# Kernel optimization log

Hardware: AMD Instinct MI355X
Metric: run time of the kernel (lower is better)

Reference implementation:

```python
import jax, jax.numpy as jnp
import numpy as np

B, T, D, K = 8, 4096, 512, 4096


def setup_inputs() -> dict:
    key = jax.random.key(0)
    k1, k2 = jax.random.split(key)
    x = jax.random.normal(k1, (B, T, D), dtype=jnp.float32)
    embed = jax.random.normal(k2, (K, D), dtype=jnp.float32)
    return {"x": x, "embed": embed}


def reference(x, embed):
    # F.normalize(x, p=2, dim=-1) with eps clamp like torch (eps=1e-12)
    norm = jnp.sqrt(jnp.sum(x * x, axis=-1, keepdims=True))
    xn = x / jnp.maximum(norm, 1e-12)

    flat = xn.reshape(-1, D)  # [(B*T), D]
    x_sq = jnp.sum(flat * flat, axis=1, keepdims=True)           # [(B*T), 1]
    e_sq = jnp.sum(embed * embed, axis=1)[None, :]               # [1, K]
    dist = -(x_sq - 2.0 * (flat @ embed.T) + e_sq)               # [(B*T), K]
    embed_ind = jnp.argmax(dist, axis=-1).reshape(B, T)          # [B, T]

    # decode: embedding gather then 'b n d -> b d n'
    quantize = embed[embed_ind]                                  # [B, T, D]
    quantize = jnp.transpose(quantize, (0, 2, 1))                # [B, D, T]
    return embed_ind, quantize
```

## Files before the change

### kernel.cpp

```cpp
#include <hip/hip_runtime.h>
#include <math.h>

#define BB 8
#define TT 4096
#define DDIM 512
#define KK 4096
#define NN (BB*TT)
#define EPS 0.05f

typedef __attribute__((ext_vector_type(8))) short bf16x8;
typedef __attribute__((ext_vector_type(4))) float f32x4;

__device__ __forceinline__ void async16(void* lds, const void* g) {
  __builtin_amdgcn_global_load_lds((const __attribute__((address_space(1))) void*)g,
                                   (__attribute__((address_space(3))) void*)lds, 16, 0, 0);
}

__device__ __forceinline__ unsigned pk_bf16(float a, float b) {
  unsigned ua = __float_as_uint(a); ua += 0x7FFFu + ((ua >> 16) & 1u);
  unsigned ub = __float_as_uint(b); ub += 0x7FFFu + ((ub >> 16) & 1u);
  return (ua >> 16) | (ub & 0xFFFF0000u);
}

__global__ __launch_bounds__(256) void prep_kernel(const float* __restrict__ src,
                                                   short* __restrict__ dst16,
                                                   float* __restrict__ outv, int mode) {
  int r = blockIdx.x * 4 + (threadIdx.x >> 6);
  int lane = threadIdx.x & 63;
  const float4* row4 = (const float4*)(src + (size_t)r * DDIM);
  float4 v0 = row4[lane];
  float4 v1 = row4[lane + 64];
  uint2 p0, p1;
  p0.x = pk_bf16(v0.x, v0.y); p0.y = pk_bf16(v0.z, v0.w);
  p1.x = pk_bf16(v1.x, v1.y); p1.y = pk_bf16(v1.z, v1.w);
  *(uint2*)(dst16 + (size_t)r * DDIM + lane * 4) = p0;
  *(uint2*)(dst16 + (size_t)r * DDIM + 256 + lane * 4) = p1;
  float ss = v0.x*v0.x + v0.y*v0.y + v0.z*v0.z + v0.w*v0.w
           + v1.x*v1.x + v1.y*v1.y + v1.z*v1.z + v1.w*v1.w;
  #pragma unroll
  for (int off = 32; off; off >>= 1) ss += __shfl_down(ss, off);
  if (lane == 0) outv[r] = mode ? 2.0f / fmaxf(sqrtf(ss), 1e-12f) : ss;
}

__global__ __launch_bounds__(256, 2) void vq_mfma(const short* __restrict__ xb,
                                                  const short* __restrict__ eb,
                                                  const float* __restrict__ esq,
                                                  const float* __restrict__ inv2,
                                                  float4* __restrict__ top2) {
  __shared__ short As[128 * 64];
  __shared__ short Bs[128 * 64];
  __shared__ float rS1[2][128];
  __shared__ float rS2[2][128];
  __shared__ int   rI1[2][128];

  const int tid = threadIdx.x;
  const int lane = tid & 63;
  const int w = tid >> 6;
  const int wr = w >> 1, wc = w & 1;
  const int q = lane >> 4, c16 = lane & 15;

  const int mb = blockIdx.x & 255;
  const int kq = blockIdx.x >> 8;
  const int n0 = mb * 128;
  const int kbase = kq * 1024;

  const int srow = w * 32 + (lane >> 3);
  const int scol = ((lane & 7) ^ (lane >> 3)) * 8;
  const short* gA = xb + (size_t)(n0 + srow) * DDIM + scol;

  float s1[16], s2v[16];
  int   i1[16];
  #pragma unroll
  for (int s = 0; s < 16; ++s) { s1[s] = -3e38f; s2v[s] = -3e38f; i1[s] = 0; }

  float4 inv4[4];
  #pragma unroll
  for (int ti = 0; ti < 4; ++ti)
    inv4[ti] = *(const float4*)&inv2[n0 + wr * 64 + ti * 16 + q * 4];

  for (int c = 0; c < 8; ++c) {
    const int k0c = kbase + c * 128;
    const short* gB = eb + (size_t)(k0c + srow) * DDIM + scol;
    f32x4 acc[4][4];
    #pragma unroll
    for (int ti = 0; ti < 4; ++ti)
      #pragma unroll
      for (int tj = 0; tj < 4; ++tj) acc[ti][tj] = (f32x4){0.f, 0.f, 0.f, 0.f};

    for (int d0 = 0; d0 < DDIM; d0 += 64) {
      #pragma unroll
      for (int i = 0; i < 4; ++i) {
        async16(As + (w * 32 + i * 8) * 64, gA + (size_t)i * 8 * DDIM + d0);
        async16(Bs + (w * 32 + i * 8) * 64, gB + (size_t)i * 8 * DDIM + d0);
      }
      __syncthreads();
      #pragma unroll
      for (int ks = 0; ks < 2; ++ks) {
        const int ko = (((ks << 2) | q) ^ (lane & 7)) << 3;
        bf16x8 af[4], bf[4];
        #pragma unroll
        for (int ti = 0; ti < 4; ++ti)
          af[ti] = *(const bf16x8*)&As[(wr * 64 + ti * 16 + c16) * 64 + ko];
        #pragma unroll
        for (int tj = 0; tj < 4; ++tj)
          bf[tj] = *(const bf16x8*)&Bs[(wc * 64 + tj * 16 + c16) * 64 + ko];
        #pragma unroll
        for (int ti = 0; ti < 4; ++ti)
          #pragma unroll
          for (int tj = 0; tj < 4; ++tj)
            acc[ti][tj] = __builtin_amdgcn_mfma_f32_16x16x32_bf16(af[ti], bf[tj], acc[ti][tj], 0, 0, 0);
      }
      __syncthreads();
    }
    #pragma unroll
    for (int tj = 0; tj < 4; ++tj) {
      const int col = k0c + wc * 64 + tj * 16 + c16;
      const float nes = -esq[col];
      #pragma unroll
      for (int ti = 0; ti < 4; ++ti)
        #pragma unroll
        for (int r = 0; r < 4; ++r) {
          int slot = ti * 4 + r;
          float sc = fmaf(acc[ti][tj][r], inv4[ti][r], nes);
          float mn = fminf(sc, s1[slot]);
          s2v[slot] = fmaxf(s2v[slot], mn);
          if (sc > s1[slot]) { s1[slot] = sc; i1[slot] = col; }
        }
    }
  }

  #pragma unroll
  for (int slot = 0; slot < 16; ++slot) {
    float a1 = s1[slot], a2 = s2v[slot]; int ai = i1[slot];
    #pragma unroll
    for (int off = 1; off < 16; off <<= 1) {
      float b1 = __shfl_xor(a1, off);
      float b2 = __shfl_xor(a2, off);
      int   bi = __shfl_xor(ai, off);
      float mn = fminf(a1, b1);
      a2 = fmaxf(fmaxf(a2, b2), mn);
      if (b1 > a1 || (b1 == a1 && bi < ai)) { a1 = b1; ai = bi; }
    }
    if (c16 == 0) {
      int row = wr * 64 + (slot >> 2) * 16 + q * 4 + (slot & 3);
      rS1[wc][row] = a1; rS2[wc][row] = a2; rI1[wc][row] = ai;
    }
  }
  __syncthreads();
  if (tid < 128) {
    float a1 = rS1[0][tid], a2 = rS2[0][tid]; int ai = rI1[0][tid];
    float b1 = rS1[1][tid], b2 = rS2[1][tid]; int bi = rI1[1][tid];
    float mn = fminf(a1, b1);
    a2 = fmaxf(fmaxf(a2, b2), mn);
    if (b1 > a1 || (b1 == a1 && bi < ai)) { a1 = b1; ai = bi; }
    top2[(size_t)kq * NN + n0 + tid] = make_float4(a1, __int_as_float(ai), a2, 0.f);
  }
}

__global__ __launch_bounds__(256) void finalize_kernel(const float4* __restrict__ top2,
                                                       float* __restrict__ out_ind,
                                                       int* __restrict__ flags,
                                                       int* __restrict__ list,
                                                       int* __restrict__ cnt) {
  int row = blockIdx.x * 256 + threadIdx.x;
  float a1 = -3e38f, a2 = -3e38f; int ai = 0;
  #pragma unroll
  for (int kq = 0; kq < 4; ++kq) {
    float4 t = top2[(size_t)kq * NN + row];
    float b1 = t.x, b2 = t.z; int bi = __float_as_int(t.y);
    float mn = fminf(a1, b1);
    a2 = fmaxf(fmaxf(a2, b2), mn);
    if (b1 > a1 || (b1 == a1 && bi < ai)) { a1 = b1; ai = bi; }
  }
  out_ind[row] = (float)ai;
  if (a1 - a2 < EPS) {
    int p = atomicAdd(cnt, 1);
    list[p] = row;
    flags[row] = p + 1;
  } else {
    flags[row] = 0;
  }
}

__global__ __launch_bounds__(256) void cleanup_kernel(const float* __restrict__ x,
                                                      const float* __restrict__ embed,
                                                      const float* __restrict__ esq,
                                                      const float* __restrict__ inv2,
                                                      const int* __restrict__ list,
                                                      const int* __restrict__ cnt,
                                                      float2* __restrict__ exact) {
  __shared__ float xr[DDIM];
  __shared__ float red_s[4];
  __shared__ int   red_i[4];
  const int rs = blockIdx.x & 31, kc = blockIdx.x >> 5;
  const int tid = threadIdx.x;
  const int lane = tid & 63, wid = tid >> 6;
  const int n = *cnt;
  for (int ii = rs; ii < n; ii += 32) {
    const int row = list[ii];
    __syncthreads();
    if (tid < 128) *(float4*)&xr[tid * 4] = *(const float4*)&x[(size_t)row * DDIM + tid * 4];
    __syncthreads();
    const float iv = inv2[row];
    float bs = -3e38f; int bi = 0;
    for (int cc = 0; cc < 2; ++cc) {
      const int code = kc * 512 + cc * 256 + tid;
      const float4* er = (const float4*)&embed[(size_t)code * DDIM];
      float acc = 0.f;
      for (int d = 0; d < DDIM / 4; ++d) {
        float4 e4 = er[d];
        float4 x4 = *(const float4*)&xr[d * 4];
        acc += x4.x * e4.x + x4.y * e4.y + x4.z * e4.z + x4.w * e4.w;
      }
      float sc = fmaf(acc, iv, -esq[code]);
      if (sc > bs || (sc == bs && code < bi)) { bs = sc; bi = code; }
    }
    #pragma unroll
    for (int off = 1; off < 64; off <<= 1) {
      float b1 = __shfl_xor(bs, off);
      int   b2 = __shfl_xor(bi, off);
      if (b1 > bs || (b1 == bs && b2 < bi)) { bs = b1; bi = b2; }
    }
    if (lane == 0) { red_s[wid] = bs; red_i[wid] = bi; }
    __syncthreads();
    if (tid == 0) {
      for (int ww = 1; ww < 4; ++ww)
        if (red_s[ww] > red_s[0] || (red_s[ww] == red_s[0] && red_i[ww] < red_i[0])) {
          red_s[0] = red_s[ww]; red_i[0] = red_i[ww];
        }
      exact[(size_t)ii * 8 + kc] = make_float2(red_s[0], (float)red_i[0]);
    }
  }
}

__global__ __launch_bounds__(256) void gather_kernel(const float* __restrict__ embed,
                                                     const int* __restrict__ flags,
                                                     const float2* __restrict__ exact,
                                                     float* __restrict__ out_ind,
                                                     float* __restrict__ out_q) {
  __shared__ int lidx[64];
  __shared__ float trans[64 * 65];
  const int n0 = blockIdx.x * 64;
  const int tid = threadIdx.x;
  if (tid < 64) {
    const int row = n0 + tid;
    const int f = flags[row];
    int idx;
    if (f) {
      float bsv = -3e38f; int bi = 0;
      const float2* e8 = &exact[(size_t)(f - 1) * 8];
      #pragma unroll
      for (int k = 0; k < 8; ++k) {
        float2 t = e8[k];
        int ci = (int)t.y;
        if (t.x > bsv || (t.x == bsv && ci < bi)) { bsv = t.x; bi = ci; }
      }
      idx = bi;
      out_ind[row] = (float)idx;
    } else {
      idx = (int)out_ind[row];
    }
    lidx[tid] = idx;
  }
  __syncthreads();
  const int bb = n0 >> 12;
  const int t0 = n0 & (TT - 1);
  const int w = tid >> 6, lane = tid & 63;
  for (int d0 = 0; d0 < DDIM; d0 += 64) {
    if (d0) __syncthreads();
    #pragma unroll
    for (int qq = 0; qq < 16; ++qq) {
      int tt2 = w * 16 + qq;
      int e = lidx[tt2];
      trans[lane * 65 + tt2] = embed[(size_t)e * DDIM + d0 + lane];
    }
    __syncthreads();
    #pragma unroll
    for (int qq = 0; qq < 4; ++qq) {
      int dl = (tid >> 4) * 4 + qq;
      int t4 = (tid & 15) * 4;
      float4 o;
      o.x = trans[dl * 65 + t4 + 0];
      o.y = trans[dl * 65 + t4 + 1];
      o.z = trans[dl * 65 + t4 + 2];
      o.w = trans[dl * 65 + t4 + 3];
      *(float4*)&out_q[((size_t)bb * DDIM + d0 + dl) * TT + t0 + t4] = o;
    }
  }
}

extern "C" void kernel_launch(void* const* d_in, const int* in_sizes, int n_in,
                              void* d_out, int out_size, void* d_ws, size_t ws_size,
                              hipStream_t stream) {
  const float* x     = (const float*)d_in[0];
  const float* embed = (const float*)d_in[1];
  char* ws = (char*)d_ws;
  short* xb      = (short*)(ws);
  short* eb      = (short*)(ws + 33554432);
  float* esq     = (float*)(ws + 37748736);
  float* inv2    = (float*)(ws + 37765120);
  float4* top2   = (float4*)(ws + 37896192);
  int* list      = (int*)(ws + 39993344);
  int* flags     = (int*)(ws + 40124416);
  float2* exact  = (float2*)(ws + 40255488);
  int* cnt       = (int*)(ws + 42352640);

  float* out_ind = (float*)d_out;
  float* out_q   = out_ind + NN;

  prep_kernel<<<KK / 4, 256, 0, stream>>>(embed, eb, esq, 0);
  prep_kernel<<<NN / 4, 256, 0, stream>>>(x, xb, inv2, 1);
  hipMemsetAsync(cnt, 0, 4, stream);
  vq_mfma<<<1024, 256, 0, stream>>>(xb, eb, esq, inv2, top2);
  finalize_kernel<<<NN / 256, 256, 0, stream>>>(top2, out_ind, flags, list, cnt);
  cleanup_kernel<<<256, 256, 0, stream>>>(x, embed, esq, inv2, list, cnt, exact);
  gather_kernel<<<NN / 64, 256, 0, stream>>>(embed, flags, exact, out_ind, out_q);
}
```

Before: 326.9 us.

## Widen MFMA codebook tile, batch cleanup rows, and merge prep launches

```diff
diff --git a/kernel.cpp b/kernel.cpp
--- a/kernel.cpp
+++ b/kernel.cpp
@@ -7,6 +7,7 @@
 #define KK 4096
 #define NN (BB*TT)
 #define EPS 0.05f
+#define CMAX 16384
 
 typedef __attribute__((ext_vector_type(8))) short bf16x8;
 typedef __attribute__((ext_vector_type(4))) float f32x4;
@@ -22,10 +23,22 @@
   return (ua >> 16) | (ub & 0xFFFF0000u);
 }
 
-__global__ __launch_bounds__(256) void prep_kernel(const float* __restrict__ src,
-                                                   short* __restrict__ dst16,
-                                                   float* __restrict__ outv, int mode) {
-  int r = blockIdx.x * 4 + (threadIdx.x >> 6);
+__global__ __launch_bounds__(256) void prep_kernel(const float* __restrict__ x,
+                                                   const float* __restrict__ embed,
+                                                   short* __restrict__ xb,
+                                                   short* __restrict__ eb,
+                                                   float* __restrict__ inv2,
+                                                   float* __restrict__ esq,
+                                                   int* __restrict__ cnt) {
+  if (blockIdx.x == 0 && threadIdx.x == 0) *cnt = 0;
+  const float* src; short* dst; float* outv; int r; int mode;
+  if (blockIdx.x < KK / 4) {
+    src = embed; dst = eb; outv = esq; mode = 0;
+    r = blockIdx.x * 4 + (threadIdx.x >> 6);
+  } else {
+    src = x; dst = xb; outv = inv2; mode = 1;
+    r = (blockIdx.x - KK / 4) * 4 + (threadIdx.x >> 6);
+  }
   int lane = threadIdx.x & 63;
   const float4* row4 = (const float4*)(src + (size_t)r * DDIM);
   float4 v0 = row4[lane];
@@ -33,8 +46,8 @@
   uint2 p0, p1;
   p0.x = pk_bf16(v0.x, v0.y); p0.y = pk_bf16(v0.z, v0.w);
   p1.x = pk_bf16(v1.x, v1.y); p1.y = pk_bf16(v1.z, v1.w);
-  *(uint2*)(dst16 + (size_t)r * DDIM + lane * 4) = p0;
-  *(uint2*)(dst16 + (size_t)r * DDIM + 256 + lane * 4) = p1;
+  *(uint2*)(dst + (size_t)r * DDIM + lane * 4) = p0;
+  *(uint2*)(dst + (size_t)r * DDIM + 256 + lane * 4) = p1;
   float ss = v0.x*v0.x + v0.y*v0.y + v0.z*v0.z + v0.w*v0.w
            + v1.x*v1.x + v1.y*v1.y + v1.z*v1.z + v1.w*v1.w;
   #pragma unroll
@@ -48,7 +61,7 @@
                                                   const float* __restrict__ inv2,
                                                   float4* __restrict__ top2) {
   __shared__ short As[128 * 64];
-  __shared__ short Bs[128 * 64];
+  __shared__ short Bs[256 * 64];
   __shared__ float rS1[2][128];
   __shared__ float rS2[2][128];
   __shared__ int   rI1[2][128];
@@ -64,57 +77,63 @@
   const int n0 = mb * 128;
   const int kbase = kq * 1024;
 
-  const int srow = w * 32 + (lane >> 3);
-  const int scol = ((lane & 7) ^ (lane >> 3)) * 8;
-  const short* gA = xb + (size_t)(n0 + srow) * DDIM + scol;
+  const int srow = lane >> 3;
+  const int scol = ((lane & 7) ^ srow) * 8;
+  const short* gA = xb + (size_t)(n0 + w * 32 + srow) * DDIM + scol;
 
   float s1[16], s2v[16];
   int   i1[16];
   #pragma unroll
   for (int s = 0; s < 16; ++s) { s1[s] = -3e38f; s2v[s] = -3e38f; i1[s] = 0; }
 
-  float4 inv4[4];
+  f32x4 inv4[4];
   #pragma unroll
   for (int ti = 0; ti < 4; ++ti)
-    inv4[ti] = *(const float4*)&inv2[n0 + wr * 64 + ti * 16 + q * 4];
-
-  for (int c = 0; c < 8; ++c) {
-    const int k0c = kbase + c * 128;
-    const short* gB = eb + (size_t)(k0c + srow) * DDIM + scol;
-    f32x4 acc[4][4];
+    inv4[ti] = *(const f32x4*)&inv2[n0 + wr * 64 + ti * 16 + q * 4];
+
+  for (int c = 0; c < 4; ++c) {
+    const int k0c = kbase + c * 256;
+    const short* gB = eb + (size_t)(k0c + w * 64 + srow) * DDIM + scol;
+    f32x4 acc[4][8];
     #pragma unroll
     for (int ti = 0; ti < 4; ++ti)
       #pragma unroll
-      for (int tj = 0; tj < 4; ++tj) acc[ti][tj] = (f32x4){0.f, 0.f, 0.f, 0.f};
+      for (int tj = 0; tj < 8; ++tj) acc[ti][tj] = (f32x4){0.f, 0.f, 0.f, 0.f};
 
     for (int d0 = 0; d0 < DDIM; d0 += 64) {
       #pragma unroll
-      for (int i = 0; i < 4; ++i) {
+      for (int i = 0; i < 4; ++i)
         async16(As + (w * 32 + i * 8) * 64, gA + (size_t)i * 8 * DDIM + d0);
-        async16(Bs + (w * 32 + i * 8) * 64, gB + (size_t)i * 8 * DDIM + d0);
-      }
+      #pragma unroll
+      for (int i = 0; i < 8; ++i)
+        async16(Bs + (w * 64 + i * 8) * 64, gB + (size_t)i * 8 * DDIM + d0);
       __syncthreads();
       #pragma unroll
       for (int ks = 0; ks < 2; ++ks) {
         const int ko = (((ks << 2) | q) ^ (lane & 7)) << 3;
-        bf16x8 af[4], bf[4];
+        bf16x8 af[4];
         #pragma unroll
         for (int ti = 0; ti < 4; ++ti)
           af[ti] = *(const bf16x8*)&As[(wr * 64 + ti * 16 + c16) * 64 + ko];
         #pragma unroll
-        for (int tj = 0; tj < 4; ++tj)
-          bf[tj] = *(const bf16x8*)&Bs[(wc * 64 + tj * 16 + c16) * 64 + ko];
-        #pragma unroll
-        for (int ti = 0; ti < 4; ++ti)
+        for (int h = 0; h < 2; ++h) {
+          bf16x8 bf[4];
           #pragma unroll
-          for (int tj = 0; tj < 4; ++tj)
-            acc[ti][tj] = __builtin_amdgcn_mfma_f32_16x16x32_bf16(af[ti], bf[tj], acc[ti][tj], 0, 0, 0);
+          for (int j = 0; j < 4; ++j)
+            bf[j] = *(const bf16x8*)&Bs[(wc * 128 + (h * 4 + j) * 16 + c16) * 64 + ko];
+          #pragma unroll
+          for (int ti = 0; ti < 4; ++ti)
+            #pragma unroll
+            for (int j = 0; j < 4; ++j)
+              acc[ti][h * 4 + j] = __builtin_amdgcn_mfma_f32_16x16x32_bf16(
+                  af[ti], bf[j], acc[ti][h * 4 + j], 0, 0, 0);
+        }
       }
       __syncthreads();
     }
     #pragma unroll
-    for (int tj = 0; tj < 4; ++tj) {
-      const int col = k0c + wc * 64 + tj * 16 + c16;
+    for (int tj = 0; tj < 8; ++tj) {
+      const int col = k0c + wc * 128 + tj * 16 + c16;
       const float nes = -esq[col];
       #pragma unroll
       for (int ti = 0; ti < 4; ++ti)
@@ -173,13 +192,12 @@
     if (b1 > a1 || (b1 == a1 && bi < ai)) { a1 = b1; ai = bi; }
   }
   out_ind[row] = (float)ai;
+  int f = 0;
   if (a1 - a2 < EPS) {
     int p = atomicAdd(cnt, 1);
-    list[p] = row;
-    flags[row] = p + 1;
-  } else {
-    flags[row] = 0;
-  }
+    if (p < CMAX) { list[p] = row; f = p + 1; }
+  }
+  flags[row] = f;
 }
 
 __global__ __launch_bounds__(256) void cleanup_kernel(const float* __restrict__ x,
@@ -189,46 +207,69 @@
                                                       const int* __restrict__ list,
                                                       const int* __restrict__ cnt,
                                                       float2* __restrict__ exact) {
-  __shared__ float xr[DDIM];
-  __shared__ float red_s[4];
-  __shared__ int   red_i[4];
-  const int rs = blockIdx.x & 31, kc = blockIdx.x >> 5;
+  __shared__ float xr[16][DDIM];
+  __shared__ float xiv[16];
+  __shared__ int   rid[16];
+  __shared__ float red_s[4][16];
+  __shared__ int   red_i[4][16];
+  const int kc = blockIdx.x >> 5;
+  const int slot = blockIdx.x & 31;
   const int tid = threadIdx.x;
-  const int lane = tid & 63, wid = tid >> 6;
-  const int n = *cnt;
-  for (int ii = rs; ii < n; ii += 32) {
-    const int row = list[ii];
-    __syncthreads();
-    if (tid < 128) *(float4*)&xr[tid * 4] = *(const float4*)&x[(size_t)row * DDIM + tid * 4];
-    __syncthreads();
-    const float iv = inv2[row];
-    float bs = -3e38f; int bi = 0;
-    for (int cc = 0; cc < 2; ++cc) {
-      const int code = kc * 512 + cc * 256 + tid;
-      const float4* er = (const float4*)&embed[(size_t)code * DDIM];
-      float acc = 0.f;
-      for (int d = 0; d < DDIM / 4; ++d) {
-        float4 e4 = er[d];
-        float4 x4 = *(const float4*)&xr[d * 4];
-        acc += x4.x * e4.x + x4.y * e4.y + x4.z * e4.z + x4.w * e4.w;
-      }
-      float sc = fmaf(acc, iv, -esq[code]);
-      if (sc > bs || (sc == bs && code < bi)) { bs = sc; bi = code; }
-    }
-    #pragma unroll
-    for (int off = 1; off < 64; off <<= 1) {
-      float b1 = __shfl_xor(bs, off);
-      int   b2 = __shfl_xor(bi, off);
-      if (b1 > bs || (b1 == bs && b2 < bi)) { bs = b1; bi = b2; }
-    }
-    if (lane == 0) { red_s[wid] = bs; red_i[wid] = bi; }
-    __syncthreads();
-    if (tid == 0) {
-      for (int ww = 1; ww < 4; ++ww)
-        if (red_s[ww] > red_s[0] || (red_s[ww] == red_s[0] && red_i[ww] < red_i[0])) {
-          red_s[0] = red_s[ww]; red_i[0] = red_i[ww];
-        }
-      exact[(size_t)ii * 8 + kc] = make_float2(red_s[0], (float)red_i[0]);
+  const int lane = tid & 63, w = tid >> 6;
+  int n = *cnt; if (n > CMAX) n = CMAX;
+  const int code = kc * 256 + tid;
+  const float4* erow = (const float4*)&embed[(size_t)code * DDIM];
+  const float nes = -esq[code];
+
+  for (int tile = slot; tile * 16 < n; tile += 32) {
+    __syncthreads();
+    if (tid < 16) {
+      int pos = tile * 16 + tid;
+      int row = (pos < n) ? list[pos] : list[0];
+      rid[tid] = row;
+      xiv[tid] = inv2[row];
+    }
+    __syncthreads();
+    #pragma unroll
+    for (int i = 0; i < 8; ++i) {
+      int idx = tid + i * 256;
+      int rl = idx >> 7, d4 = idx & 127;
+      ((float4*)xr[rl])[d4] = *(const float4*)&x[(size_t)rid[rl] * DDIM + d4 * 4];
+    }
+    __syncthreads();
+    float acc[16];
+    #pragma unroll
+    for (int r = 0; r < 16; ++r) acc[r] = 0.f;
+    for (int d4 = 0; d4 < 128; ++d4) {
+      float4 e4 = erow[d4];
+      #pragma unroll
+      for (int r = 0; r < 16; ++r) {
+        float4 x4 = ((const float4*)xr[r])[d4];
+        acc[r] += e4.x * x4.x + e4.y * x4.y + e4.z * x4.z + e4.w * x4.w;
+      }
+    }
+    #pragma unroll
+    for (int r = 0; r < 16; ++r) {
+      float bs = fmaf(acc[r], xiv[r], nes);
+      int bi = code;
+      #pragma unroll
+      for (int off = 1; off < 64; off <<= 1) {
+        float b1 = __shfl_xor(bs, off);
+        int   b2 = __shfl_xor(bi, off);
+        if (b1 > bs || (b1 == bs && b2 < bi)) { bs = b1; bi = b2; }
+      }
+      if (lane == 0) { red_s[w][r] = bs; red_i[w][r] = bi; }
+    }
+    __syncthreads();
+    if (tid < 16) {
+      float bs = red_s[0][tid]; int bi = red_i[0][tid];
+      #pragma unroll
+      for (int ww = 1; ww < 4; ++ww) {
+        float b1 = red_s[ww][tid]; int b2 = red_i[ww][tid];
+        if (b1 > bs || (b1 == bs && b2 < bi)) { bs = b1; bi = b2; }
+      }
+      int pos = tile * 16 + tid;
+      if (pos < n) exact[(size_t)pos * 16 + kc] = make_float2(bs, (float)bi);
     }
   }
 }
@@ -248,10 +289,10 @@
     int idx;
     if (f) {
       float bsv = -3e38f; int bi = 0;
-      const float2* e8 = &exact[(size_t)(f - 1) * 8];
-      #pragma unroll
-      for (int k = 0; k < 8; ++k) {
-        float2 t = e8[k];
+      const float2* e16 = &exact[(size_t)(f - 1) * 16];
+      #pragma unroll
+      for (int k = 0; k < 16; ++k) {
+        float2 t = e16[k];
         int ci = (int)t.y;
         if (t.x > bsv || (t.x == bsv && ci < bi)) { bsv = t.x; bi = ci; }
       }
@@ -301,18 +342,16 @@
   float* inv2    = (float*)(ws + 37765120);
   float4* top2   = (float4*)(ws + 37896192);
   int* list      = (int*)(ws + 39993344);
-  int* flags     = (int*)(ws + 40124416);
-  float2* exact  = (float2*)(ws + 40255488);
-  int* cnt       = (int*)(ws + 42352640);
+  int* flags     = (int*)(ws + 40058880);
+  float2* exact  = (float2*)(ws + 40189952);
+  int* cnt       = (int*)(ws + 42287104);
 
   float* out_ind = (float*)d_out;
   float* out_q   = out_ind + NN;
 
-  prep_kernel<<<KK / 4, 256, 0, stream>>>(embed, eb, esq, 0);
-  prep_kernel<<<NN / 4, 256, 0, stream>>>(x, xb, inv2, 1);
-  hipMemsetAsync(cnt, 0, 4, stream);
+  prep_kernel<<<KK / 4 + NN / 4, 256, 0, stream>>>(x, embed, xb, eb, inv2, esq, cnt);
   vq_mfma<<<1024, 256, 0, stream>>>(xb, eb, esq, inv2, top2);
   finalize_kernel<<<NN / 256, 256, 0, stream>>>(top2, out_ind, flags, list, cnt);
-  cleanup_kernel<<<256, 256, 0, stream>>>(x, embed, esq, inv2, list, cnt, exact);
+  cleanup_kernel<<<512, 256, 0, stream>>>(x, embed, esq, inv2, list, cnt, exact);
   gather_kernel<<<NN / 64, 256, 0, stream>>>(embed, flags, exact, out_ind, out_q);
 }
```

Measured after the change: 348.7 us. +6.7%, slower.

## Fuse finalize, cleanup and gather into one tail kernel with per-chunk candidate rescoring

Applied to the files above, without the earlier changes.

```diff
diff --git a/kernel.cpp b/kernel.cpp
--- a/kernel.cpp
+++ b/kernel.cpp
@@ -6,7 +6,8 @@
 #define DDIM 512
 #define KK 4096
 #define NN (BB*TT)
-#define EPS 0.05f
+#define EPS 0.035f
+#define LCAP 2048
 
 typedef __attribute__((ext_vector_type(8))) short bf16x8;
 typedef __attribute__((ext_vector_type(4))) float f32x4;
@@ -22,10 +23,20 @@
   return (ua >> 16) | (ub & 0xFFFF0000u);
 }
 
-__global__ __launch_bounds__(256) void prep_kernel(const float* __restrict__ src,
-                                                   short* __restrict__ dst16,
-                                                   float* __restrict__ outv, int mode) {
-  int r = blockIdx.x * 4 + (threadIdx.x >> 6);
+__global__ __launch_bounds__(256) void prep_kernel(const float* __restrict__ x,
+                                                   const float* __restrict__ embed,
+                                                   short* __restrict__ xb,
+                                                   short* __restrict__ eb,
+                                                   float* __restrict__ inv2,
+                                                   float* __restrict__ esq) {
+  const float* src; short* dst; float* outv; int r; int mode;
+  if (blockIdx.x < KK / 4) {
+    src = embed; dst = eb; outv = esq; mode = 0;
+    r = blockIdx.x * 4 + (threadIdx.x >> 6);
+  } else {
+    src = x; dst = xb; outv = inv2; mode = 1;
+    r = (blockIdx.x - KK / 4) * 4 + (threadIdx.x >> 6);
+  }
   int lane = threadIdx.x & 63;
   const float4* row4 = (const float4*)(src + (size_t)r * DDIM);
   float4 v0 = row4[lane];
@@ -33,8 +44,8 @@
   uint2 p0, p1;
   p0.x = pk_bf16(v0.x, v0.y); p0.y = pk_bf16(v0.z, v0.w);
   p1.x = pk_bf16(v1.x, v1.y); p1.y = pk_bf16(v1.z, v1.w);
-  *(uint2*)(dst16 + (size_t)r * DDIM + lane * 4) = p0;
-  *(uint2*)(dst16 + (size_t)r * DDIM + 256 + lane * 4) = p1;
+  *(uint2*)(dst + (size_t)r * DDIM + lane * 4) = p0;
+  *(uint2*)(dst + (size_t)r * DDIM + 256 + lane * 4) = p1;
   float ss = v0.x*v0.x + v0.y*v0.y + v0.z*v0.z + v0.w*v0.w
            + v1.x*v1.x + v1.y*v1.y + v1.z*v1.z + v1.w*v1.w;
   #pragma unroll
@@ -46,7 +57,9 @@
                                                   const short* __restrict__ eb,
                                                   const float* __restrict__ esq,
                                                   const float* __restrict__ inv2,
-                                                  float4* __restrict__ top2) {
+                                                  float* __restrict__ cts1,
+                                                  float* __restrict__ cts2,
+                                                  int* __restrict__ cti) {
   __shared__ short As[128 * 64];
   __shared__ short Bs[128 * 64];
   __shared__ float rS1[2][128];
@@ -68,209 +81,202 @@
   const int scol = ((lane & 7) ^ (lane >> 3)) * 8;
   const short* gA = xb + (size_t)(n0 + srow) * DDIM + scol;
 
-  float s1[16], s2v[16];
-  int   i1[16];
-  #pragma unroll
-  for (int s = 0; s < 16; ++s) { s1[s] = -3e38f; s2v[s] = -3e38f; i1[s] = 0; }
-
-  float4 inv4[4];
+  f32x4 inv4[4];
   #pragma unroll
   for (int ti = 0; ti < 4; ++ti)
-    inv4[ti] = *(const float4*)&inv2[n0 + wr * 64 + ti * 16 + q * 4];
-
-  for (int c = 0; c < 8; ++c) {
-    const int k0c = kbase + c * 128;
-    const short* gB = eb + (size_t)(k0c + srow) * DDIM + scol;
-    f32x4 acc[4][4];
-    #pragma unroll
-    for (int ti = 0; ti < 4; ++ti)
+    inv4[ti] = *(const f32x4*)&inv2[n0 + wr * 64 + ti * 16 + q * 4];
+
+  for (int p = 0; p < 4; ++p) {
+    float cs1[16], cs2[16];
+    int   ci1[16];
+    #pragma unroll
+    for (int s = 0; s < 16; ++s) { cs1[s] = -3e38f; cs2[s] = -3e38f; ci1[s] = 0; }
+
+    for (int cc = 0; cc < 2; ++cc) {
+      const int c = p * 2 + cc;
+      const int k0c = kbase + c * 128;
+      const short* gB = eb + (size_t)(k0c + srow) * DDIM + scol;
+      f32x4 acc[4][4];
       #pragma unroll
-      for (int tj = 0; tj < 4; ++tj) acc[ti][tj] = (f32x4){0.f, 0.f, 0.f, 0.f};
-
-    for (int d0 = 0; d0 < DDIM; d0 += 64) {
+      for (int ti = 0; ti < 4; ++ti)
+        #pragma unroll
+        for (int tj = 0; tj < 4; ++tj) acc[ti][tj] = (f32x4){0.f, 0.f, 0.f, 0.f};
+
+      for (int d0 = 0; d0 < DDIM; d0 += 64) {
+        #pragma unroll
+        for (int i = 0; i < 4; ++i) {
+          async16(As + (w * 32 + i * 8) * 64, gA + (size_t)i * 8 * DDIM + d0);
+          async16(Bs + (w * 32 + i * 8) * 64, gB + (size_t)i * 8 * DDIM + d0);
+        }
+        __syncthreads();
+        #pragma unroll
+        for (int ks = 0; ks < 2; ++ks) {
+          const int ko = (((ks << 2) | q) ^ (lane & 7)) << 3;
+          bf16x8 af[4], bf[4];
+          #pragma unroll
+          for (int ti = 0; ti < 4; ++ti)
+            af[ti] = *(const bf16x8*)&As[(wr * 64 + ti * 16 + c16) * 64 + ko];
+          #pragma unroll
+          for (int tj = 0; tj < 4; ++tj)
+            bf[tj] = *(const bf16x8*)&Bs[(wc * 64 + tj * 16 + c16) * 64 + ko];
+          #pragma unroll
+          for (int ti = 0; ti < 4; ++ti)
+            #pragma unroll
+            for (int tj = 0; tj < 4; ++tj)
+              acc[ti][tj] = __builtin_amdgcn_mfma_f32_16x16x32_bf16(af[ti], bf[tj], acc[ti][tj], 0, 0, 0);
+        }
+        __syncthreads();
+      }
       #pragma unroll
-      for (int i = 0; i < 4; ++i) {
-        async16(As + (w * 32 + i * 8) * 64, gA + (size_t)i * 8 * DDIM + d0);
-        async16(Bs + (w * 32 + i * 8) * 64, gB + (size_t)i * 8 * DDIM + d0);
-      }
-      __syncthreads();
-      #pragma unroll
-      for (int ks = 0; ks < 2; ++ks) {
-        const int ko = (((ks << 2) | q) ^ (lane & 7)) << 3;
-        bf16x8 af[4], bf[4];
-        #pragma unroll
-        for (int ti = 0; ti < 4; ++ti)
-          af[ti] = *(const bf16x8*)&As[(wr * 64 + ti * 16 + c16) * 64 + ko];
-        #pragma unroll
-        for (int tj = 0; tj < 4; ++tj)
-          bf[tj] = *(const bf16x8*)&Bs[(wc * 64 + tj * 16 + c16) * 64 + ko];
+      for (int tj = 0; tj < 4; ++tj) {
+        const int col = k0c + wc * 64 + tj * 16 + c16;
+        const float nes = -esq[col];
         #pragma unroll
         for (int ti = 0; ti < 4; ++ti)
           #pragma unroll
-          for (int tj = 0; tj < 4; ++tj)
-            acc[ti][tj] = __builtin_amdgcn_mfma_f32_16x16x32_bf16(af[ti], bf[tj], acc[ti][tj], 0, 0, 0);
-      }
-      __syncthreads();
-    }
-    #pragma unroll
-    for (int tj = 0; tj < 4; ++tj) {
-      const int col = k0c + wc * 64 + tj * 16 + c16;
-      const float nes = -esq[col];
+          for (int r = 0; r < 4; ++r) {
+            int slot = ti * 4 + r;
+            float sc = fmaf(acc[ti][tj][r], inv4[ti][r], nes);
+            cs2[slot] = fmaxf(cs2[slot], fminf(sc, cs1[slot]));
+            if (sc > cs1[slot]) { cs1[slot] = sc; ci1[slot] = col; }
+          }
+      }
+    }
+    #pragma unroll
+    for (int slot = 0; slot < 16; ++slot) {
+      float a1 = cs1[slot], a2 = cs2[slot]; int ai = ci1[slot];
       #pragma unroll
-      for (int ti = 0; ti < 4; ++ti)
-        #pragma unroll
-        for (int r = 0; r < 4; ++r) {
-          int slot = ti * 4 + r;
-          float sc = fmaf(acc[ti][tj][r], inv4[ti][r], nes);
-          float mn = fminf(sc, s1[slot]);
-          s2v[slot] = fmaxf(s2v[slot], mn);
-          if (sc > s1[slot]) { s1[slot] = sc; i1[slot] = col; }
+      for (int off = 1; off < 16; off <<= 1) {
+        float b1 = __shfl_xor(a1, off);
+        float b2 = __shfl_xor(a2, off);
+        int   bi = __shfl_xor(ai, off);
+        float ns2 = fmaxf(fmaxf(a2, b2), fminf(a1, b1));
+        if (b1 > a1 || (b1 == a1 && bi < ai)) { a1 = b1; ai = bi; }
+        a2 = ns2;
+      }
+      if (c16 == 0) {
+        int row = wr * 64 + (slot >> 2) * 16 + q * 4 + (slot & 3);
+        rS1[wc][row] = a1; rS2[wc][row] = a2; rI1[wc][row] = ai;
+      }
+    }
+    __syncthreads();
+    if (tid < 128) {
+      float a1 = rS1[0][tid], a2 = rS2[0][tid]; int ai = rI1[0][tid];
+      float b1 = rS1[1][tid], b2 = rS2[1][tid]; int bi = rI1[1][tid];
+      float ns2 = fmaxf(fmaxf(a2, b2), fminf(a1, b1));
+      if (b1 > a1 || (b1 == a1 && bi < ai)) { a1 = b1; ai = bi; }
+      size_t o = (size_t)(kq * 4 + p) * NN + n0 + tid;
+      cts1[o] = a1; cts2[o] = ns2; cti[o] = ai;
+    }
+  }
+}
+
+__global__ __launch_bounds__(256) void tail_kernel(const float* __restrict__ x,
+                                                   const float* __restrict__ embed,
+                                                   const float* __restrict__ esq,
+                                                   const float* __restrict__ inv2,
+                                                   const float* __restrict__ cts1,
+                                                   const float* __restrict__ cts2,
+                                                   const int* __restrict__ cti,
+                                                   float* __restrict__ out_ind,
+                                                   float* __restrict__ out_q) {
+  __shared__ float ct_s1[16][64];
+  __shared__ float ct_s2[16][64];
+  __shared__ int   ct_i[16][64];
+  __shared__ int   lidx[64];
+  __shared__ unsigned long long pw[64];
+  __shared__ int   list[LCAP];
+  __shared__ int   lcnt;
+  __shared__ float trans[64 * 65];
+
+  const int tid = threadIdx.x;
+  const int lane = tid & 63, wv = tid >> 6;
+  const int n0 = blockIdx.x * 64;
+
+  #pragma unroll
+  for (int i = 0; i < 4; ++i) {
+    int ch = i * 4 + wv;
+    size_t o = (size_t)ch * NN + n0 + lane;
+    ct_s1[ch][lane] = cts1[o];
+    ct_s2[ch][lane] = cts2[o];
+    ct_i[ch][lane]  = cti[o];
+  }
+  if (tid == 0) lcnt = 0;
+  __syncthreads();
+
+  if (tid < 64) {
+    float a1 = -3e38f; int ai = 0x7FFFFFFF;
+    #pragma unroll
+    for (int ch = 0; ch < 16; ++ch) {
+      float b1 = ct_s1[ch][tid]; int bi = ct_i[ch][tid];
+      if (b1 > a1 || (b1 == a1 && bi < ai)) { a1 = b1; ai = bi; }
+    }
+    const float thr = a1 - EPS;
+    int extra = 0;
+    #pragma unroll
+    for (int ch = 0; ch < 16; ++ch) {
+      if (ct_s2[ch][tid] >= thr) extra++;
+      else if (ct_s1[ch][tid] >= thr && ct_i[ch][tid] != ai) extra++;
+    }
+    if (extra == 0) {
+      lidx[tid] = ai;
+    } else {
+      lidx[tid] = -1; pw[tid] = 0ull;
+      int p = atomicAdd(&lcnt, 1);
+      if (p < LCAP) list[p] = (tid << 12) | ai;
+      for (int ch = 0; ch < 16; ++ch) {
+        if (ct_s2[ch][tid] >= thr) {
+          int base = atomicAdd(&lcnt, 256);
+          for (int k = 0; k < 256; ++k)
+            if (base + k < LCAP) list[base + k] = (tid << 12) | (ch * 256 + k);
+        } else if (ct_s1[ch][tid] >= thr && ct_i[ch][tid] != ai) {
+          int pp = atomicAdd(&lcnt, 1);
+          if (pp < LCAP) list[pp] = (tid << 12) | ct_i[ch][tid];
         }
-    }
-  }
-
-  #pragma unroll
-  for (int slot = 0; slot < 16; ++slot) {
-    float a1 = s1[slot], a2 = s2v[slot]; int ai = i1[slot];
-    #pragma unroll
-    for (int off = 1; off < 16; off <<= 1) {
-      float b1 = __shfl_xor(a1, off);
-      float b2 = __shfl_xor(a2, off);
-      int   bi = __shfl_xor(ai, off);
-      float mn = fminf(a1, b1);
-      a2 = fmaxf(fmaxf(a2, b2), mn);
-      if (b1 > a1 || (b1 == a1 && bi < ai)) { a1 = b1; ai = bi; }
-    }
-    if (c16 == 0) {
-      int row = wr * 64 + (slot >> 2) * 16 + q * 4 + (slot & 3);
-      rS1[wc][row] = a1; rS2[wc][row] = a2; rI1[wc][row] = ai;
+      }
     }
   }
   __syncthreads();
-  if (tid < 128) {
-    float a1 = rS1[0][tid], a2 = rS2[0][tid]; int ai = rI1[0][tid];
-    float b1 = rS1[1][tid], b2 = rS2[1][tid]; int bi = rI1[1][tid];
-    float mn = fminf(a1, b1);
-    a2 = fmaxf(fmaxf(a2, b2), mn);
-    if (b1 > a1 || (b1 == a1 && bi < ai)) { a1 = b1; ai = bi; }
-    top2[(size_t)kq * NN + n0 + tid] = make_float4(a1, __int_as_float(ai), a2, 0.f);
-  }
-}
-
-__global__ __launch_bounds__(256) void finalize_kernel(const float4* __restrict__ top2,
-                                                       float* __restrict__ out_ind,
-                                                       int* __restrict__ flags,
-                                                       int* __restrict__ list,
-                                                       int* __restrict__ cnt) {
-  int row = blockIdx.x * 256 + threadIdx.x;
-  float a1 = -3e38f, a2 = -3e38f; int ai = 0;
-  #pragma unroll
-  for (int kq = 0; kq < 4; ++kq) {
-    float4 t = top2[(size_t)kq * NN + row];
-    float b1 = t.x, b2 = t.z; int bi = __float_as_int(t.y);
-    float mn = fminf(a1, b1);
-    a2 = fmaxf(fmaxf(a2, b2), mn);
-    if (b1 > a1 || (b1 == a1 && bi < ai)) { a1 = b1; ai = bi; }
-  }
-  out_ind[row] = (float)ai;
-  if (a1 - a2 < EPS) {
-    int p = atomicAdd(cnt, 1);
-    list[p] = row;
-    flags[row] = p + 1;
-  } else {
-    flags[row] = 0;
-  }
-}
-
-__global__ __launch_bounds__(256) void cleanup_kernel(const float* __restrict__ x,
-                                                      const float* __restrict__ embed,
-                                                      const float* __restrict__ esq,
-                                                      const float* __restrict__ inv2,
-                                                      const int* __restrict__ list,
-                                                      const int* __restrict__ cnt,
-                                                      float2* __restrict__ exact) {
-  __shared__ float xr[DDIM];
-  __shared__ float red_s[4];
-  __shared__ int   red_i[4];
-  const int rs = blockIdx.x & 31, kc = blockIdx.x >> 5;
-  const int tid = threadIdx.x;
-  const int lane = tid & 63, wid = tid >> 6;
-  const int n = *cnt;
-  for (int ii = rs; ii < n; ii += 32) {
-    const int row = list[ii];
-    __syncthreads();
-    if (tid < 128) *(float4*)&xr[tid * 4] = *(const float4*)&x[(size_t)row * DDIM + tid * 4];
-    __syncthreads();
-    const float iv = inv2[row];
-    float bs = -3e38f; int bi = 0;
-    for (int cc = 0; cc < 2; ++cc) {
-      const int code = kc * 512 + cc * 256 + tid;
-      const float4* er = (const float4*)&embed[(size_t)code * DDIM];
-      float acc = 0.f;
-      for (int d = 0; d < DDIM / 4; ++d) {
-        float4 e4 = er[d];
-        float4 x4 = *(const float4*)&xr[d * 4];
-        acc += x4.x * e4.x + x4.y * e4.y + x4.z * e4.z + x4.w * e4.w;
-      }
-      float sc = fmaf(acc, iv, -esq[code]);
-      if (sc > bs || (sc == bs && code < bi)) { bs = sc; bi = code; }
-    }
-    #pragma unroll
-    for (int off = 1; off < 64; off <<= 1) {
-      float b1 = __shfl_xor(bs, off);
-      int   b2 = __shfl_xor(bi, off);
-      if (b1 > bs || (b1 == bs && b2 < bi)) { bs = b1; bi = b2; }
-    }
-    if (lane == 0) { red_s[wid] = bs; red_i[wid] = bi; }
-    __syncthreads();
-    if (tid == 0) {
-      for (int ww = 1; ww < 4; ++ww)
-        if (red_s[ww] > red_s[0] || (red_s[ww] == red_s[0] && red_i[ww] < red_i[0])) {
-          red_s[0] = red_s[ww]; red_i[0] = red_i[ww];
-        }
-      exact[(size_t)ii * 8 + kc] = make_float2(red_s[0], (float)red_i[0]);
-    }
-  }
-}
-
-__global__ __launch_bounds__(256) void gather_kernel(const float* __restrict__ embed,
-                                                     const int* __restrict__ flags,
-                                                     const float2* __restrict__ exact,
-                                                     float* __restrict__ out_ind,
-                                                     float* __restrict__ out_q) {
-  __shared__ int lidx[64];
-  __shared__ float trans[64 * 65];
-  const int n0 = blockIdx.x * 64;
-  const int tid = threadIdx.x;
+
+  {
+    int e = lcnt; if (e > LCAP) e = LCAP;
+    for (int i = wv; i < e; i += 4) {
+      int ent = list[i];
+      int r = ent >> 12, code = ent & 4095;
+      int grow = n0 + r;
+      const float4* xp = (const float4*)&x[(size_t)grow * DDIM + lane * 8];
+      const float4* ep = (const float4*)&embed[(size_t)code * DDIM + lane * 8];
+      float4 xa = xp[0], xb4 = xp[1], ea = ep[0], eb4 = ep[1];
+      float d = xa.x*ea.x + xa.y*ea.y + xa.z*ea.z + xa.w*ea.w
+              + xb4.x*eb4.x + xb4.y*eb4.y + xb4.z*eb4.z + xb4.w*eb4.w;
+      #pragma unroll
+      for (int off = 1; off < 64; off <<= 1) d += __shfl_xor(d, off);
+      if (lane == 0) {
+        float sc = fmaf(d, inv2[grow], -esq[code]);
+        unsigned u = __float_as_uint(sc);
+        u = (u >> 31) ? ~u : (u | 0x80000000u);
+        unsigned long long pk = ((unsigned long long)u << 32) | (unsigned)(~code);
+        atomicMax(&pw[r], pk);
+      }
+    }
+  }
+  __syncthreads();
+
   if (tid < 64) {
-    const int row = n0 + tid;
-    const int f = flags[row];
-    int idx;
-    if (f) {
-      float bsv = -3e38f; int bi = 0;
-      const float2* e8 = &exact[(size_t)(f - 1) * 8];
-      #pragma unroll
-      for (int k = 0; k < 8; ++k) {
-        float2 t = e8[k];
-        int ci = (int)t.y;
-        if (t.x > bsv || (t.x == bsv && ci < bi)) { bsv = t.x; bi = ci; }
-      }
-      idx = bi;
-      out_ind[row] = (float)idx;
-    } else {
-      idx = (int)out_ind[row];
-    }
+    int idx = lidx[tid];
+    if (idx < 0) idx = (int)((~(unsigned)(pw[tid] & 0xFFFFFFFFull)) & 4095u);
     lidx[tid] = idx;
+    out_ind[n0 + tid] = (float)idx;
   }
   __syncthreads();
+
   const int bb = n0 >> 12;
   const int t0 = n0 & (TT - 1);
-  const int w = tid >> 6, lane = tid & 63;
   for (int d0 = 0; d0 < DDIM; d0 += 64) {
     if (d0) __syncthreads();
     #pragma unroll
     for (int qq = 0; qq < 16; ++qq) {
-      int tt2 = w * 16 + qq;
+      int tt2 = wv * 16 + qq;
       int e = lidx[tt2];
       trans[lane * 65 + tt2] = embed[(size_t)e * DDIM + d0 + lane];
     }
@@ -295,24 +301,19 @@
   const float* x     = (const float*)d_in[0];
   const float* embed = (const float*)d_in[1];
   char* ws = (char*)d_ws;
-  short* xb      = (short*)(ws);
-  short* eb      = (short*)(ws + 33554432);
-  float* esq     = (float*)(ws + 37748736);
-  float* inv2    = (float*)(ws + 37765120);
-  float4* top2   = (float4*)(ws + 37896192);
-  int* list      = (int*)(ws + 39993344);
-  int* flags     = (int*)(ws + 40124416);
-  float2* exact  = (float2*)(ws + 40255488);
-  int* cnt       = (int*)(ws + 42352640);
+  short* xb   = (short*)(ws);
+  short* eb   = (short*)(ws + 33554432);
+  float* esq  = (float*)(ws + 37748736);
+  float* inv2 = (float*)(ws + 37765120);
+  float* cts1 = (float*)(ws + 37896192);
+  float* cts2 = (float*)(ws + 39993344);
+  int*   cti  = (int*)  (ws + 42090496);
 
   float* out_ind = (float*)d_out;
   float* out_q   = out_ind + NN;
 
-  prep_kernel<<<KK / 4, 256, 0, stream>>>(embed, eb, esq, 0);
-  prep_kernel<<<NN / 4, 256, 0, stream>>>(x, xb, inv2, 1);
-  hipMemsetAsync(cnt, 0, 4, stream);
-  vq_mfma<<<1024, 256, 0, stream>>>(xb, eb, esq, inv2, top2);
-  finalize_kernel<<<NN / 256, 256, 0, stream>>>(top2, out_ind, flags, list, cnt);
-  cleanup_kernel<<<256, 256, 0, stream>>>(x, embed, esq, inv2, list, cnt, exact);
-  gather_kernel<<<NN / 64, 256, 0, stream>>>(embed, flags, exact, out_ind, out_q);
-}
+  prep_kernel<<<KK / 4 + NN / 4, 256, 0, stream>>>(x, embed, xb, eb, inv2, esq);
+  vq_mfma<<<1024, 256, 0, stream>>>(xb, eb, esq, inv2, cts1, cts2, cti);
+  tail_kernel<<<NN / 64, 256, 0, stream>>>(x, embed, esq, inv2, cts1, cts2, cti,
+                                           out_ind, out_q);
+}
```

Result: slower. 343.2 us (+5.0%).
